# Optimization experiments

Measured on AMD Instinct MI355X. Metric: run time of the kernel, lower is better.

The kernel has to match this reference:

```python
import jax, jax.numpy as jnp
import numpy as np

N_FREQS = 6  # PositionEmbedding N_freqs when embedding=='pe'

def _pe(x):
    freqs = (2.0 ** jnp.arange(N_FREQS)).astype(x.dtype)
    fx = x * freqs  # [B,Q,N_FREQS]
    sc = jnp.stack([jnp.sin(fx), jnp.cos(fx)], axis=-1).reshape(fx.shape[0], fx.shape[1], 2 * N_FREQS)
    return jnp.concatenate([x, sc], axis=-1)

def _mlp(h, W1, b1, W2, b2, W3, b3):
    h = jax.nn.relu(h @ W1 + b1)
    h = jax.nn.relu(h @ W2 + b2)
    return h @ W3 + b3

def setup_inputs() -> dict:
    key = jax.random.key(0)
    B, Q, N, D, H = 4, 65536, 8192, 16, 128
    ks = jax.random.split(key, 6)
    coord = jax.random.uniform(ks[0], (B, Q, 1), minval=-1.0, maxval=1.0, dtype=jnp.float32)
    latent = jax.random.normal(ks[1], (B, N, D), dtype=jnp.float32)
    in_dim = (1 + 2 * N_FREQS) + 3 * D  # pe(rel_coord) ++ unfolded feat = 13 + 48 = 61
    def init(k, shp, fan):
        return (jax.random.normal(k, shp, dtype=jnp.float32) / np.float32(np.sqrt(fan)))
    W1 = init(ks[2], (in_dim, H), in_dim); b1 = jnp.zeros((H,), jnp.float32)
    W2 = init(ks[3], (H, H), H);          b2 = jnp.zeros((H,), jnp.float32)
    W3 = init(ks[4], (H, 1), H);          b3 = jnp.zeros((1,), jnp.float32)
    return dict(coord=coord, latent=latent, W1=W1, b1=b1, W2=W2, b2=b2, W3=W3, b3=b3)

def reference(coord, latent, W1, b1, W2, b2, W3, b3):
    B, Q, _ = coord.shape
    N = latent.shape[1]
    # feat_unfold: concat shifted-prev / self / shifted-next along feature dim -> [B,N,3D]
    prev = jnp.concatenate([latent[:, :1], latent[:, :-1]], axis=1)
    nxt = jnp.concatenate([latent[:, 1:], latent[:, -1:]], axis=1)
    feat = jnp.concatenate([prev, latent, nxt], axis=-1)
    # make_coord grid: cell centers in [-1,1]
    grid = (-1.0 + (2.0 * jnp.arange(N, dtype=coord.dtype) + 1.0) / N)
    rx = 1.0 / N           # 2/num_latents/2
    eps_shift = 1e-6
    preds, areas = [], []
    for vx in (-2.0, 0.0):  # eval path vx_lst
        c = jnp.clip(coord + vx * rx + eps_shift, -1.0 + 1e-6, 1.0 - 1e-6)
        idx = jnp.clip(jnp.searchsorted(grid, c[..., 0]), 0, N - 1)  # [B,Q]
        q_coord = grid[idx][..., None]                               # [B,Q,1]
        q_feat = jnp.take_along_axis(feat, idx[..., None], axis=1)   # [B,Q,3D]
        rel = (coord - q_coord) * N                                  # scaled rel coord
        area = jnp.abs(rel[..., 0]) + 1e-9                           # [B,Q]
        inp = jnp.concatenate([_pe(rel), q_feat], axis=-1)           # [B,Q,61]
        preds.append(_mlp(inp, W1, b1, W2, b2, W3, b3))              # [B,Q,1]
        areas.append(area)
    tot = areas[0] + areas[1]
    # local_ensemble: swap areas before weighting
    ret = preds[0] * (areas[1] / tot)[..., None] + preds[1] * (areas[0] / tot)[..., None]
    return ret
```

## Files before the change

kernel.cpp:

```cpp
#include <hip/hip_runtime.h>
#include <hip/hip_bf16.h>

typedef short s8v __attribute__((ext_vector_type(8)));
typedef float f4v __attribute__((ext_vector_type(4)));
typedef unsigned u4v __attribute__((ext_vector_type(4)));

__device__ __forceinline__ unsigned short f2bf(float x) {
  unsigned u = __builtin_bit_cast(unsigned, x);
  u += 0x7fffu + ((u >> 16) & 1u);
  return (unsigned short)(u >> 16);
}
__device__ __forceinline__ unsigned pk2(float a, float b) {
  unsigned ua = __builtin_bit_cast(unsigned, a) + 0x8000u;
  unsigned ub = __builtin_bit_cast(unsigned, b) + 0x8000u;
  return __builtin_amdgcn_perm(ub, ua, 0x07060302u);
}

__global__ void prep_kernel(const float* __restrict__ W1, const float* __restrict__ b1,
                            const float* __restrict__ W2, unsigned short* __restrict__ wsW) {
  int e = blockIdx.x * 256 + threadIdx.x;
  if (e < 8192) {
    int frag = e >> 9, rem = e & 511, lane = rem >> 3, j = rem & 7;
    int h = frag >> 1, ks = frag & 1;
    int q4 = lane >> 4, l15 = lane & 15;
    int k = ks * 32 + q4 * 8 + j;
    int n = h * 16 + l15;
    float v;
    if (k < 13) v = W1[k * 128 + n];
    else if (k == 13) v = b1[n];
    else if (k < 16) v = 0.0f;
    else v = W1[(k - 3) * 128 + n];
    wsW[e] = f2bf(v);
  } else {
    int e2 = e - 8192;
    int frag = e2 >> 9, rem = e2 & 511, lane = rem >> 3, j = rem & 7;
    int h2 = frag >> 2, ks = frag & 3;
    int q4 = lane >> 4, l15 = lane & 15;
    int kd = (j < 4) ? (32 * ks + 4 * q4 + j) : (32 * ks + 16 + 4 * q4 + (j - 4));
    int n = h2 * 16 + l15;
    wsW[e] = f2bf(W2[kd * 128 + n]);
  }
}

__global__ __launch_bounds__(128, 2) void lisagon_main(
    const float* __restrict__ coord, const float* __restrict__ latent,
    const unsigned short* __restrict__ W1f, const unsigned short* __restrict__ W2f,
    const float* __restrict__ b2, const float* __restrict__ W3,
    const float* __restrict__ b3, float* __restrict__ out) {
  __shared__ __align__(16) unsigned short A1[128 * 64];
  __shared__ float AREA[128];

  const int t = threadIdx.x;
  const int lane = t & 63, wv = t >> 6;
  const int l15 = lane & 15, q4 = lane >> 4;

  {
    const int r = t;
    const int Rg = blockIdx.x * 128 + r;
    const int gq = Rg >> 1, p = Rg & 1;
    const float co = coord[gq];
    float c = (co + (p ? 0.0f : -0.000244140625f)) + 1e-6f;
    c = fminf(fmaxf(c, -1.0f + 1e-6f), 1.0f - 1e-6f);
    double u = ((double)c * 8192.0 + 8191.0) * 0.5;
    int idx = (int)ceil(u);
    idx = min(max(idx, 0), 8191);

    float qc = ((float)(2 * idx + 1) - 8192.0f) * (1.0f / 8192.0f);
    float rel = (co - qc) * 8192.0f;
    AREA[r] = fabsf(rel) + 1e-9f;

    uint4* A1v = (uint4*)A1;
    const float4* latv = (const float4*)(latent + (size_t)(gq >> 16) * (8192 * 16));
    int rows3[3];
    rows3[0] = max(idx - 1, 0);
    rows3[1] = idx;
    rows3[2] = min(idx + 1, 8191);
    float4 L[3][4];
#pragma unroll
    for (int s = 0; s < 3; s++)
#pragma unroll
      for (int w = 0; w < 4; w++) L[s][w] = latv[rows3[s] * 4 + w];

    float v[16];
    v[0] = rel;
    float f = rel;
#pragma unroll
    for (int i = 0; i < 6; i++) {
      v[1 + 2 * i] = __sinf(f);
      v[2 + 2 * i] = __cosf(f);
      f = f + f;
    }
    v[13] = 1.0f;
    v[14] = 0.0f; v[15] = 0.0f;
#pragma unroll
    for (int ch = 0; ch < 2; ch++) {
      union { uint4 u4; unsigned us[4]; } pkv;
#pragma unroll
      for (int w = 0; w < 4; w++) pkv.us[w] = pk2(v[ch * 8 + 2 * w], v[ch * 8 + 2 * w + 1]);
      A1v[r * 8 + (ch ^ (r & 7))] = pkv.u4;
    }
#pragma unroll
    for (int s = 0; s < 3; s++) {
      union { uint4 u4; unsigned us[4]; } p0, p1;
      p0.us[0] = pk2(L[s][0].x, L[s][0].y); p0.us[1] = pk2(L[s][0].z, L[s][0].w);
      p0.us[2] = pk2(L[s][1].x, L[s][1].y); p0.us[3] = pk2(L[s][1].z, L[s][1].w);
      p1.us[0] = pk2(L[s][2].x, L[s][2].y); p1.us[1] = pk2(L[s][2].z, L[s][2].w);
      p1.us[2] = pk2(L[s][3].x, L[s][3].y); p1.us[3] = pk2(L[s][3].z, L[s][3].w);
      int ch0 = 2 + 2 * s;
      A1v[r * 8 + (ch0 ^ (r & 7))]       = p0.u4;
      A1v[r * 8 + ((ch0 + 1) ^ (r & 7))] = p1.u4;
    }
  }
  __syncthreads();

  const s8v* W1fv = (const s8v*)W1f;
  const s8v* W2fv = (const s8v*)W2f;
  const s8v* A1s  = (const s8v*)A1;
  const int rbase = wv * 64;

  s8v Bf[2][4];
#pragma unroll
  for (int ks = 0; ks < 2; ks++)
#pragma unroll
    for (int rt = 0; rt < 4; rt++) {
      int row = rbase + rt * 16 + l15;
      Bf[ks][rt] = A1s[row * 8 + ((ks * 4 + q4) ^ (row & 7))];
    }

  u4v bbv[4][4];
#pragma unroll
  for (int h = 0; h < 8; h++) {
    f4v a[4];
#pragma unroll
    for (int rt = 0; rt < 4; rt++) a[rt] = (f4v){0.f, 0.f, 0.f, 0.f};
#pragma unroll
    for (int ks = 0; ks < 2; ks++) {
      s8v Af = W1fv[(h * 2 + ks) * 64 + lane];
#pragma unroll
      for (int rt = 0; rt < 4; rt++)
        a[rt] = __builtin_amdgcn_mfma_f32_16x16x32_bf16(Af, Bf[ks][rt], a[rt], 0, 0, 0);
    }
#pragma unroll
    for (int rt = 0; rt < 4; rt++) {
      bbv[rt][h >> 1][2 * (h & 1)]     = pk2(fmaxf(a[rt][0], 0.f), fmaxf(a[rt][1], 0.f));
      bbv[rt][h >> 1][2 * (h & 1) + 1] = pk2(fmaxf(a[rt][2], 0.f), fmaxf(a[rt][3], 0.f));
    }
  }

  float s[4] = {0.f, 0.f, 0.f, 0.f};
#pragma unroll
  for (int h2 = 0; h2 < 8; h2++) {
    f4v a2[4];
    f4v b2v = ((const f4v*)b2)[h2 * 4 + q4];
#pragma unroll
    for (int rt = 0; rt < 4; rt++) a2[rt] = b2v;
#pragma unroll
    for (int ks = 0; ks < 4; ks++) {
      s8v Af = W2fv[(h2 * 4 + ks) * 64 + lane];
#pragma unroll
      for (int rt = 0; rt < 4; rt++)
        a2[rt] = __builtin_amdgcn_mfma_f32_16x16x32_bf16(
            Af, __builtin_bit_cast(s8v, bbv[rt][ks]), a2[rt], 0, 0, 0);
    }
    float4 w3v = ((const float4*)W3)[h2 * 4 + q4];
#pragma unroll
    for (int rt = 0; rt < 4; rt++) {
      s[rt] += fmaxf(a2[rt][0], 0.f) * w3v.x;
      s[rt] += fmaxf(a2[rt][1], 0.f) * w3v.y;
      s[rt] += fmaxf(a2[rt][2], 0.f) * w3v.z;
      s[rt] += fmaxf(a2[rt][3], 0.f) * w3v.w;
    }
  }

  const float b3s = b3[0];
#pragma unroll
  for (int rt = 0; rt < 4; rt++) {
    float pred = s[rt];
    pred += __shfl_xor(pred, 16, 64);
    pred += __shfl_xor(pred, 32, 64);
    pred += b3s;
    float other = __shfl_xor(pred, 1, 64);
    if (q4 == 0 && (l15 & 1) == 0) {
      int row0 = rbase + rt * 16 + l15;
      float a0 = AREA[row0], a1 = AREA[row0 + 1];
      float tot = a0 + a1;
      out[(blockIdx.x * 128 + row0) >> 1] = pred * (a1 / tot) + other * (a0 / tot);
    }
  }
}

extern "C" void kernel_launch(void* const* d_in, const int* in_sizes, int n_in,
                              void* d_out, int out_size, void* d_ws, size_t ws_size,
                              hipStream_t stream) {
  const float* coord  = (const float*)d_in[0];
  const float* latent = (const float*)d_in[1];
  const float* W1 = (const float*)d_in[2];
  const float* b1 = (const float*)d_in[3];
  const float* W2 = (const float*)d_in[4];
  const float* b2 = (const float*)d_in[5];
  const float* W3 = (const float*)d_in[6];
  const float* b3 = (const float*)d_in[7];
  float* out = (float*)d_out;
  unsigned short* wsW = (unsigned short*)d_ws;

  prep_kernel<<<96, 256, 0, stream>>>(W1, b1, W2, wsW);
  lisagon_main<<<4096, 128, 0, stream>>>(coord, latent, wsW, wsW + 8192,
                                         b2, W3, b3, out);
}
```

Baseline: 103.9 us.

## Halve rows per block and split gather work across two waves

Each block now handles 64 rows instead of 128, and the grid doubles to 8192 blocks. The prologue is split by wave: one wave computes the positional encoding and gathers the previous latent row, while the other gathers the current and next rows. Each wave then does MFMA on 32 rows instead of 64. This is meant to spread the gather latency and cut per-thread register pressure, at the cost of loading the weight fragments twice as often per row.

```diff
diff --git a/kernel.cpp b/kernel.cpp
--- a/kernel.cpp
+++ b/kernel.cpp
@@ -47,16 +47,17 @@
     const unsigned short* __restrict__ W1f, const unsigned short* __restrict__ W2f,
     const float* __restrict__ b2, const float* __restrict__ W3,
     const float* __restrict__ b3, float* __restrict__ out) {
-  __shared__ __align__(16) unsigned short A1[128 * 64];
-  __shared__ float AREA[128];
+  __shared__ __align__(16) unsigned short A1[64 * 64];
+  __shared__ float AREA[64];
 
   const int t = threadIdx.x;
   const int lane = t & 63, wv = t >> 6;
   const int l15 = lane & 15, q4 = lane >> 4;
 
   {
-    const int r = t;
-    const int Rg = blockIdx.x * 128 + r;
+    const int r = t & 63;
+    const int role = t >> 6;
+    const int Rg = blockIdx.x * 64 + r;
     const int gq = Rg >> 1, p = Rg & 1;
     const float co = coord[gq];
     float c = (co + (p ? 0.0f : -0.000244140625f)) + 1e-6f;
@@ -65,50 +66,60 @@
     int idx = (int)ceil(u);
     idx = min(max(idx, 0), 8191);
 
-    float qc = ((float)(2 * idx + 1) - 8192.0f) * (1.0f / 8192.0f);
-    float rel = (co - qc) * 8192.0f;
-    AREA[r] = fabsf(rel) + 1e-9f;
-
     uint4* A1v = (uint4*)A1;
     const float4* latv = (const float4*)(latent + (size_t)(gq >> 16) * (8192 * 16));
-    int rows3[3];
-    rows3[0] = max(idx - 1, 0);
-    rows3[1] = idx;
-    rows3[2] = min(idx + 1, 8191);
-    float4 L[3][4];
-#pragma unroll
-    for (int s = 0; s < 3; s++)
-#pragma unroll
-      for (int w = 0; w < 4; w++) L[s][w] = latv[rows3[s] * 4 + w];
-
-    float v[16];
-    v[0] = rel;
-    float f = rel;
-#pragma unroll
-    for (int i = 0; i < 6; i++) {
-      v[1 + 2 * i] = __sinf(f);
-      v[2 + 2 * i] = __cosf(f);
-      f = f + f;
-    }
-    v[13] = 1.0f;
-    v[14] = 0.0f; v[15] = 0.0f;
-#pragma unroll
-    for (int ch = 0; ch < 2; ch++) {
-      union { uint4 u4; unsigned us[4]; } pkv;
-#pragma unroll
-      for (int w = 0; w < 4; w++) pkv.us[w] = pk2(v[ch * 8 + 2 * w], v[ch * 8 + 2 * w + 1]);
-      A1v[r * 8 + (ch ^ (r & 7))] = pkv.u4;
-    }
-#pragma unroll
-    for (int s = 0; s < 3; s++) {
+
+    if (role == 0) {
+      int lr = max(idx - 1, 0);
+      float4 a = latv[lr * 4 + 0], b = latv[lr * 4 + 1];
+      float4 cc = latv[lr * 4 + 2], d = latv[lr * 4 + 3];
+
+      float qc = ((float)(2 * idx + 1) - 8192.0f) * (1.0f / 8192.0f);
+      float rel = (co - qc) * 8192.0f;
+      AREA[r] = fabsf(rel) + 1e-9f;
+      float v[16];
+      v[0] = rel;
+      float f = rel;
+#pragma unroll
+      for (int i = 0; i < 6; i++) {
+        v[1 + 2 * i] = __sinf(f);
+        v[2 + 2 * i] = __cosf(f);
+        f = f + f;
+      }
+      v[13] = 1.0f;
+      v[14] = 0.0f; v[15] = 0.0f;
+#pragma unroll
+      for (int ch = 0; ch < 2; ch++) {
+        union { uint4 u4; unsigned us[4]; } pkv;
+#pragma unroll
+        for (int w = 0; w < 4; w++) pkv.us[w] = pk2(v[ch * 8 + 2 * w], v[ch * 8 + 2 * w + 1]);
+        A1v[r * 8 + (ch ^ (r & 7))] = pkv.u4;
+      }
       union { uint4 u4; unsigned us[4]; } p0, p1;
-      p0.us[0] = pk2(L[s][0].x, L[s][0].y); p0.us[1] = pk2(L[s][0].z, L[s][0].w);
-      p0.us[2] = pk2(L[s][1].x, L[s][1].y); p0.us[3] = pk2(L[s][1].z, L[s][1].w);
-      p1.us[0] = pk2(L[s][2].x, L[s][2].y); p1.us[1] = pk2(L[s][2].z, L[s][2].w);
-      p1.us[2] = pk2(L[s][3].x, L[s][3].y); p1.us[3] = pk2(L[s][3].z, L[s][3].w);
-      int ch0 = 2 + 2 * s;
-      A1v[r * 8 + (ch0 ^ (r & 7))]       = p0.u4;
-      A1v[r * 8 + ((ch0 + 1) ^ (r & 7))] = p1.u4;
+      p0.us[0] = pk2(a.x, a.y);  p0.us[1] = pk2(a.z, a.w);
+      p0.us[2] = pk2(b.x, b.y);  p0.us[3] = pk2(b.z, b.w);
+      p1.us[0] = pk2(cc.x, cc.y); p1.us[1] = pk2(cc.z, cc.w);
+      p1.us[2] = pk2(d.x, d.y);  p1.us[3] = pk2(d.z, d.w);
+      A1v[r * 8 + (2 ^ (r & 7))] = p0.u4;
+      A1v[r * 8 + (3 ^ (r & 7))] = p1.u4;
+    } else {
+      int lr1 = min(idx + 1, 8191);
+      float4 L[2][4];
+#pragma unroll
+      for (int w = 0; w < 4; w++) L[0][w] = latv[idx * 4 + w];
+#pragma unroll
+      for (int w = 0; w < 4; w++) L[1][w] = latv[lr1 * 4 + w];
+#pragma unroll
+      for (int s = 0; s < 2; s++) {
+        union { uint4 u4; unsigned us[4]; } p0, p1;
+        p0.us[0] = pk2(L[s][0].x, L[s][0].y); p0.us[1] = pk2(L[s][0].z, L[s][0].w);
+        p0.us[2] = pk2(L[s][1].x, L[s][1].y); p0.us[3] = pk2(L[s][1].z, L[s][1].w);
+        p1.us[0] = pk2(L[s][2].x, L[s][2].y); p1.us[1] = pk2(L[s][2].z, L[s][2].w);
+        p1.us[2] = pk2(L[s][3].x, L[s][3].y); p1.us[3] = pk2(L[s][3].z, L[s][3].w);
+        int ch0 = 4 + 2 * s;
+        A1v[r * 8 + (ch0 ^ (r & 7))]       = p0.u4;
+        A1v[r * 8 + ((ch0 + 1) ^ (r & 7))] = p1.u4;
+      }
     }
   }
   __syncthreads();
@@ -116,55 +127,54 @@
   const s8v* W1fv = (const s8v*)W1f;
   const s8v* W2fv = (const s8v*)W2f;
   const s8v* A1s  = (const s8v*)A1;
-  const int rbase = wv * 64;
-
-  s8v Bf[2][4];
+  const int rbase = wv * 32;
+
+  s8v Bf[2][2];
 #pragma unroll
   for (int ks = 0; ks < 2; ks++)
 #pragma unroll
-    for (int rt = 0; rt < 4; rt++) {
+    for (int rt = 0; rt < 2; rt++) {
       int row = rbase + rt * 16 + l15;
       Bf[ks][rt] = A1s[row * 8 + ((ks * 4 + q4) ^ (row & 7))];
     }
 
-  u4v bbv[4][4];
+  u4v bbv[2][4];
 #pragma unroll
   for (int h = 0; h < 8; h++) {
-    f4v a[4];
-#pragma unroll
-    for (int rt = 0; rt < 4; rt++) a[rt] = (f4v){0.f, 0.f, 0.f, 0.f};
+    f4v a[2];
+#pragma unroll
+    for (int rt = 0; rt < 2; rt++) a[rt] = (f4v){0.f, 0.f, 0.f, 0.f};
 #pragma unroll
     for (int ks = 0; ks < 2; ks++) {
       s8v Af = W1fv[(h * 2 + ks) * 64 + lane];
 #pragma unroll
-      for (int rt = 0; rt < 4; rt++)
+      for (int rt = 0; rt < 2; rt++)
         a[rt] = __builtin_amdgcn_mfma_f32_16x16x32_bf16(Af, Bf[ks][rt], a[rt], 0, 0, 0);
     }
 #pragma unroll
-    for (int rt = 0; rt < 4; rt++) {
+    for (int rt = 0; rt < 2; rt++) {
       bbv[rt][h >> 1][2 * (h & 1)]     = pk2(fmaxf(a[rt][0], 0.f), fmaxf(a[rt][1], 0.f));
       bbv[rt][h >> 1][2 * (h & 1) + 1] = pk2(fmaxf(a[rt][2], 0.f), fmaxf(a[rt][3], 0.f));
     }
   }
 
-  float s[4] = {0.f, 0.f, 0.f, 0.f};
+  float s[2] = {0.f, 0.f};
 #pragma unroll
   for (int h2 = 0; h2 < 8; h2++) {
-    f4v a2[4];
+    f4v a2[2];
     f4v b2v = ((const f4v*)b2)[h2 * 4 + q4];
-#pragma unroll
-    for (int rt = 0; rt < 4; rt++) a2[rt] = b2v;
+    a2[0] = b2v; a2[1] = b2v;
 #pragma unroll
     for (int ks = 0; ks < 4; ks++) {
       s8v Af = W2fv[(h2 * 4 + ks) * 64 + lane];
 #pragma unroll
-      for (int rt = 0; rt < 4; rt++)
+      for (int rt = 0; rt < 2; rt++)
         a2[rt] = __builtin_amdgcn_mfma_f32_16x16x32_bf16(
             Af, __builtin_bit_cast(s8v, bbv[rt][ks]), a2[rt], 0, 0, 0);
     }
     float4 w3v = ((const float4*)W3)[h2 * 4 + q4];
 #pragma unroll
-    for (int rt = 0; rt < 4; rt++) {
+    for (int rt = 0; rt < 2; rt++) {
       s[rt] += fmaxf(a2[rt][0], 0.f) * w3v.x;
       s[rt] += fmaxf(a2[rt][1], 0.f) * w3v.y;
       s[rt] += fmaxf(a2[rt][2], 0.f) * w3v.z;
@@ -174,7 +184,7 @@
 
   const float b3s = b3[0];
 #pragma unroll
-  for (int rt = 0; rt < 4; rt++) {
+  for (int rt = 0; rt < 2; rt++) {
     float pred = s[rt];
     pred += __shfl_xor(pred, 16, 64);
     pred += __shfl_xor(pred, 32, 64);
@@ -184,7 +194,7 @@
       int row0 = rbase + rt * 16 + l15;
       float a0 = AREA[row0], a1 = AREA[row0 + 1];
       float tot = a0 + a1;
-      out[(blockIdx.x * 128 + row0) >> 1] = pred * (a1 / tot) + other * (a0 / tot);
+      out[(blockIdx.x * 64 + row0) >> 1] = pred * (a1 / tot) + other * (a0 / tot);
     }
   }
 }
@@ -204,6 +214,6 @@
   unsigned short* wsW = (unsigned short*)d_ws;
 
   prep_kernel<<<96, 256, 0, stream>>>(W1, b1, W2, wsW);
-  lisagon_main<<<4096, 128, 0, stream>>>(coord, latent, wsW, wsW + 8192,
+  lisagon_main<<<8192, 128, 0, stream>>>(coord, latent, wsW, wsW + 8192,
                                          b2, W3, b3, out);
 }
```

New measurement: 119.6 us. 15.1% more time.
